# Optimization experiments

Measured on AMD Instinct MI355X. Metric: run time of the kernel, lower is better.

## Reference

```python
import jax, jax.numpy as jnp
import numpy as np

B = 32          # number of trees (batch)
N_LEAVES = 512  # complete binary tree -> 2*N_LEAVES-1 nodes per tree
IN_DIM = 1024
MEM = 1024


def setup_inputs() -> dict:
    key = jax.random.key(0)
    k1, k2, k3, k4 = jax.random.split(key, 4)
    s = 0.02
    inputs = jax.random.normal(k1, (B, N_LEAVES, IN_DIM), jnp.float32)
    w_fioux = jax.random.normal(k2, (4 * MEM, IN_DIM), jnp.float32) * s
    # rand_init: bias zero except first mem_dim entries set to 1 (forget-gate bias)
    b_fioux = jnp.zeros((4 * MEM,), jnp.float32).at[:MEM].set(1.0)
    w_iouh = jax.random.normal(k3, (3 * MEM, 2 * MEM), jnp.float32) * s
    w_fh = jax.random.normal(k4, (2 * MEM, 2 * MEM), jnp.float32) * s
    return {"inputs": inputs, "w_fioux": w_fioux, "b_fioux": b_fioux,
            "w_iouh": w_iouh, "w_fh": w_fh}


def _node_forward(x, child_c, child_h, w_fioux, b_fioux, w_iouh, w_fh):
    # x: [B, n, IN_DIM]; child_c/child_h: [B, n, 2*MEM] (left || right)
    fioux = x @ w_fioux.T + b_fioux                      # [B, n, 4M]
    fx, ix, ox, ux = jnp.split(fioux, 4, axis=-1)        # each [B, n, M]
    ih, oh, uh = jnp.split(child_h @ w_iouh.T, 3, axis=-1)
    i = jax.nn.sigmoid(ix + ih)
    o = jax.nn.sigmoid(ox + oh)
    u = jnp.tanh(ux + uh)
    # f gates: fx repeated for both children + fh(child_h)
    f = jax.nn.sigmoid(jnp.concatenate([fx, fx], axis=-1) + child_h @ w_fh.T)
    fc = f * child_c                                     # [B, n, 2M]
    c = i * u + fc[..., :MEM] + fc[..., MEM:]            # sum over the 2 children
    h = o * jnp.tanh(c)
    return c, h


def reference(inputs, w_fioux, b_fioux, w_iouh, w_fh):
    # Leaves: x = word input, child states are zeros
    z = jnp.zeros((B, N_LEAVES, 2 * MEM), inputs.dtype)
    c, h = _node_forward(inputs, z, z, w_fioux, b_fioux, w_iouh, w_fh)
    n = N_LEAVES
    # Internal nodes, level by level (log2(N_LEAVES) fixed iterations):
    # x = zeros (internal nodes have no token input), children are adjacent pairs.
    while n > 1:
        n //= 2
        child_c = c.reshape(B, n, 2 * MEM)   # [left_c || right_c]
        child_h = h.reshape(B, n, 2 * MEM)
        x = jnp.zeros((B, n, IN_DIM), inputs.dtype)
        c, h = _node_forward(x, child_c, child_h, w_fioux, b_fioux, w_iouh, w_fh)
    return h[:, 0, :]  # root hidden state, [B, MEM]
```

## Files before the change

kernel.cpp:

```cpp
#include <hip/hip_runtime.h>
#include <cstdint>
#include <cstddef>


typedef __attribute__((ext_vector_type(8))) short bf16x8;
typedef __attribute__((ext_vector_type(4))) float f32x4;

__device__ __forceinline__ float sig_(float x) { return 1.0f / (1.0f + __expf(-x)); }

__device__ __forceinline__ unsigned short f2bf_(float x) {
    union { float f; uint32_t u; } v; v.f = x;
    uint32_t r = v.u + 0x7fffu + ((v.u >> 16) & 1u);
    return (unsigned short)(r >> 16);
}
__device__ __forceinline__ float bf2f_(unsigned short u) {
    union { uint32_t u; float f; } v; v.u = ((uint32_t)u) << 16; return v.f;
}

#define GL16(g, l) __builtin_amdgcn_global_load_lds( \
    (const __attribute__((address_space(1))) void*)(g), \
    (__attribute__((address_space(3))) void*)(l), 16, 0, 0)

__global__ __launch_bounds__(512, 2)
void gemm256(const unsigned short* __restrict__ A,
             const unsigned short* __restrict__ W,
             unsigned short* __restrict__ C, int M, int N, int lda, int Klen)
{
    __shared__ unsigned short lA[4 * 8192];
    __shared__ unsigned short lB[4 * 8192];

    const int gx = gridDim.x, gy = gridDim.y;
    int id = blockIdx.x + gx * (blockIdx.y + gy * blockIdx.z);
    {
        const int nwg = gx * gy * gridDim.z;
        const int q = nwg >> 3, r = nwg & 7, x = id & 7, i = id >> 3;
        id = (x < r ? x * (q + 1) : r * (q + 1) + (x - r) * q) + i;
    }
    const int bz  = id / (gx * gy);
    const int rem = id - bz * gx * gy;
    const int by  = rem / gx;
    const int bx  = rem - by * gx;

    const int tid = threadIdx.x;
    const int ln  = tid & 63;
    const int wv  = tid >> 6;
    const int wrp = wv >> 2;
    const int wcp = wv & 3;
    const int row0 = by * 256;
    const int colb = bx * 256;
    const int kbase = bz * Klen;
    C += (size_t)bz * M * N;

    const int rowS = tid >> 2;
    const int gS   = (tid & 3) ^ ((tid >> 3) & 3);
    const unsigned short* a0 = A + (size_t)min(row0 + rowS,       M - 1) * lda + kbase + gS * 8;
    const unsigned short* a1 = A + (size_t)min(row0 + rowS + 128, M - 1) * lda + kbase + gS * 8;
    const unsigned short* b0 = W + (size_t)(colb + rowS)       * lda + kbase + gS * 8;
    const unsigned short* b1 = W + (size_t)(colb + rowS + 128) * lda + kbase + gS * 8;
    const int ld0 = tid * 8;
    const int ld1 = tid * 8 + 4096;

    int offA[8], offB[4];
    #pragma unroll
    for (int i = 0; i < 8; ++i) {
        const int r = wrp * 128 + i * 16 + (ln & 15);
        offA[i] = r * 32 + ((ln >> 4) ^ ((r >> 1) & 3)) * 8;
    }
    #pragma unroll
    for (int i = 0; i < 4; ++i) {
        const int r = wcp * 64 + i * 16 + (ln & 15);
        offB[i] = r * 32 + ((ln >> 4) ^ ((r >> 1) & 3)) * 8;
    }

    f32x4 acc[8][4] = {};
    const int NT = Klen >> 6;

#define ISSUE_KH(kh) do { \
    const int _sl = (kh) & 3; \
    const size_t _ko = (size_t)(kh) * 32; \
    GL16(a0 + _ko, lA + _sl * 8192 + ld0); \
    GL16(a1 + _ko, lA + _sl * 8192 + ld1); \
    GL16(b0 + _ko, lB + _sl * 8192 + ld0); \
    GL16(b1 + _ko, lB + _sl * 8192 + ld1); \
} while (0)

#define PHASE(SLOT, KH, DOISS, WAITN, DOBAR) do { \
    const unsigned short* _pa = lA + (SLOT) * 8192; \
    const unsigned short* _pb = lB + (SLOT) * 8192; \
    bf16x8 _af[8], _bf[4]; \
    _Pragma("unroll") for (int _i = 0; _i < 4; ++_i) _bf[_i] = *(const bf16x8*)(_pb + offB[_i]); \
    _Pragma("unroll") for (int _i = 0; _i < 4; ++_i) _af[_i] = *(const bf16x8*)(_pa + offA[_i]); \
    if (DOISS) ISSUE_KH(KH); \
    __builtin_amdgcn_s_setprio(1); \
    _Pragma("unroll") for (int _m = 0; _m < 4; ++_m) \
        _Pragma("unroll") for (int _n = 0; _n < 4; ++_n) \
            acc[_m][_n] = __builtin_amdgcn_mfma_f32_16x16x32_bf16(_af[_m], _bf[_n], acc[_m][_n], 0, 0, 0); \
    __builtin_amdgcn_s_setprio(0); \
    _Pragma("unroll") for (int _i = 4; _i < 8; ++_i) _af[_i] = *(const bf16x8*)(_pa + offA[_i]); \
    __builtin_amdgcn_s_setprio(1); \
    _Pragma("unroll") for (int _m = 4; _m < 8; ++_m) \
        _Pragma("unroll") for (int _n = 0; _n < 4; ++_n) \
            acc[_m][_n] = __builtin_amdgcn_mfma_f32_16x16x32_bf16(_af[_m], _bf[_n], acc[_m][_n], 0, 0, 0); \
    __builtin_amdgcn_s_setprio(0); \
    if ((WAITN) == 8)      asm volatile("s_waitcnt vmcnt(8)" ::: "memory"); \
    else if ((WAITN) == 4) asm volatile("s_waitcnt vmcnt(4)" ::: "memory"); \
    else if ((WAITN) == 0) asm volatile("s_waitcnt vmcnt(0)" ::: "memory"); \
    if (DOBAR) asm volatile("s_barrier" ::: "memory"); \
} while (0)

    ISSUE_KH(0); ISSUE_KH(1); ISSUE_KH(2);
    asm volatile("s_waitcnt vmcnt(8)" ::: "memory");
    asm volatile("s_barrier" ::: "memory");

    for (int t = 0; t <= NT - 3; ++t) {
        const int ph = 2 * t;
        PHASE((ph) & 3,     ph + 3, 1, 8, 1);
        PHASE((ph + 1) & 3, ph + 4, 1, 8, 1);
    }
    {
        const int ph = 2 * NT - 4;
        PHASE((ph) & 3,     ph + 3, 1,  8, 1);
        PHASE((ph + 1) & 3, 0,      0,  4, 1);
        PHASE((ph + 2) & 3, 0,      0,  0, 1);
        PHASE((ph + 3) & 3, 0,      0, -1, 0);
    }
#undef PHASE
#undef ISSUE_KH

    #pragma unroll
    for (int mi = 0; mi < 8; ++mi) {
        #pragma unroll
        for (int ni = 0; ni < 4; ++ni) {
            const int col = colb + wcp * 64 + ni * 16 + (ln & 15);
            #pragma unroll
            for (int rg = 0; rg < 4; ++rg) {
                const int r = row0 + wrp * 128 + mi * 16 + (ln >> 4) * 4 + rg;
                if (r < M) C[(size_t)r * N + col] = f2bf_(acc[mi][ni][rg]);
            }
        }
    }
}

__global__ void f2bf_vec(const float* __restrict__ src, unsigned short* __restrict__ dst, int n4)
{
    const int i = blockIdx.x * blockDim.x + threadIdx.x;
    if (i >= n4) return;
    const float4 v = ((const float4*)src)[i];
    ushort4 o;
    o.x = f2bf_(v.x); o.y = f2bf_(v.y); o.z = f2bf_(v.z); o.w = f2bf_(v.w);
    ((ushort4*)dst)[i] = o;
}

__global__ void leaf_gates(const unsigned short* __restrict__ g, const float* __restrict__ b,
                           unsigned short* __restrict__ c_out, unsigned short* __restrict__ h_out,
                           int rows)
{
    const int idx = blockIdx.x * blockDim.x + threadIdx.x;
    if (idx >= rows * 256) return;
    const int r = idx >> 8, q = (idx & 255) << 2;
    const unsigned short* gr = g + (size_t)r * 3072;
    const ushort4 ix = *(const ushort4*)(gr + q);
    const ushort4 ox = *(const ushort4*)(gr + 1024 + q);
    const ushort4 ux = *(const ushort4*)(gr + 2048 + q);
    const float* bi = b + 1024 + q;
    const float* bo = b + 2048 + q;
    const float* bu = b + 3072 + q;
    ushort4 co, ho;
    const float c0 = sig_(bf2f_(ix.x) + bi[0]) * tanhf(bf2f_(ux.x) + bu[0]);
    const float c1 = sig_(bf2f_(ix.y) + bi[1]) * tanhf(bf2f_(ux.y) + bu[1]);
    const float c2 = sig_(bf2f_(ix.z) + bi[2]) * tanhf(bf2f_(ux.z) + bu[2]);
    const float c3 = sig_(bf2f_(ix.w) + bi[3]) * tanhf(bf2f_(ux.w) + bu[3]);
    co.x = f2bf_(c0); co.y = f2bf_(c1); co.z = f2bf_(c2); co.w = f2bf_(c3);
    ho.x = f2bf_(sig_(bf2f_(ox.x) + bo[0]) * tanhf(c0));
    ho.y = f2bf_(sig_(bf2f_(ox.y) + bo[1]) * tanhf(c1));
    ho.z = f2bf_(sig_(bf2f_(ox.z) + bo[2]) * tanhf(c2));
    ho.w = f2bf_(sig_(bf2f_(ox.w) + bo[3]) * tanhf(c3));
    *(ushort4*)(c_out + (size_t)r * 1024 + q) = co;
    *(ushort4*)(h_out + (size_t)r * 1024 + q) = ho;
}

__device__ __forceinline__ void acc4_(float* v, ushort4 u) {
    v[0] += bf2f_(u.x); v[1] += bf2f_(u.y); v[2] += bf2f_(u.z); v[3] += bf2f_(u.w);
}

__global__ void node_gates(const unsigned short* __restrict__ g, int S, size_t sstride,
                           const float* __restrict__ b,
                           const unsigned short* __restrict__ c_prev,
                           unsigned short* __restrict__ c_out,
                           unsigned short* __restrict__ h_bf,
                           float* __restrict__ h_f32, int rows)
{
    const int idx = blockIdx.x * blockDim.x + threadIdx.x;
    if (idx >= rows * 256) return;
    const int r = idx >> 8, q = (idx & 255) << 2;
    float vi[4] = {}, vo[4] = {}, vu[4] = {}, vfl[4] = {}, vfr[4] = {};
    const unsigned short* gr = g + (size_t)r * 5120 + q;
    for (int s = 0; s < S; ++s, gr += sstride) {
        acc4_(vi,  *(const ushort4*)(gr));
        acc4_(vo,  *(const ushort4*)(gr + 1024));
        acc4_(vu,  *(const ushort4*)(gr + 2048));
        acc4_(vfl, *(const ushort4*)(gr + 3072));
        acc4_(vfr, *(const ushort4*)(gr + 4096));
    }
    const float* bi = b + 1024 + q;
    const float* bo = b + 2048 + q;
    const float* bu = b + 3072 + q;
    const float* bff = b + q;
    const ushort4 clu = *(const ushort4*)(c_prev + (size_t)r * 2048 + q);
    const ushort4 cru = *(const ushort4*)(c_prev + (size_t)r * 2048 + 1024 + q);
    const float cl[4] = { bf2f_(clu.x), bf2f_(clu.y), bf2f_(clu.z), bf2f_(clu.w) };
    const float cr[4] = { bf2f_(cru.x), bf2f_(cru.y), bf2f_(cru.z), bf2f_(cru.w) };

    ushort4 co, ho;
    float hv[4];
    float cv[4];
    #pragma unroll
    for (int e = 0; e < 4; ++e) {
        const float c = sig_(vi[e] + bi[e]) * tanhf(vu[e] + bu[e])
                      + sig_(vfl[e] + bff[e]) * cl[e]
                      + sig_(vfr[e] + bff[e]) * cr[e];
        cv[e] = c;
        hv[e] = sig_(vo[e] + bo[e]) * tanhf(c);
    }
    co.x = f2bf_(cv[0]); co.y = f2bf_(cv[1]); co.z = f2bf_(cv[2]); co.w = f2bf_(cv[3]);
    ho.x = f2bf_(hv[0]); ho.y = f2bf_(hv[1]); ho.z = f2bf_(hv[2]); ho.w = f2bf_(hv[3]);
    *(ushort4*)(c_out + (size_t)r * 1024 + q) = co;
    *(ushort4*)(h_bf + (size_t)r * 1024 + q) = ho;
    if (h_f32) {
        float4 hf; hf.x = hv[0]; hf.y = hv[1]; hf.z = hv[2]; hf.w = hv[3];
        *(float4*)(h_f32 + (size_t)r * 1024 + q) = hf;
    }
}

extern "C" void kernel_launch(void* const* d_in, const int* in_sizes, int n_in,
                              void* d_out, int out_size, void* d_ws, size_t ws_size,
                              hipStream_t stream)
{
    const float* inputs  = (const float*)d_in[0];
    const float* w_fioux = (const float*)d_in[1];
    const float* b_fioux = (const float*)d_in[2];
    const float* w_iouh  = (const float*)d_in[3];
    const float* w_fh    = (const float*)d_in[4];
    float* out = (float*)d_out;

    unsigned short* us   = (unsigned short*)d_ws;
    unsigned short* c_a  = us;
    unsigned short* c_b  = c_a + (size_t)16777216;
    unsigned short* h_a  = c_b + (size_t)8388608;
    unsigned short* h_b  = h_a + (size_t)16777216;
    unsigned short* wfx  = h_b + (size_t)8388608;
    unsigned short* wcat = wfx + (size_t)3145728;
    unsigned short* gbuf = wcat + (size_t)10485760;
    unsigned short* x_bf = c_a;

    f2bf_vec<<<16384, 256, 0, stream>>>(inputs, x_bf, 4194304);
    f2bf_vec<<<3072, 256, 0, stream>>>(w_fioux + (size_t)1024 * 1024, wfx, 786432);
    f2bf_vec<<<6144, 256, 0, stream>>>(w_iouh, wcat, 1572864);
    f2bf_vec<<<4096, 256, 0, stream>>>(w_fh, wcat + (size_t)3072 * 2048, 1048576);

    gemm256<<<dim3(12, 64, 1), 512, 0, stream>>>(x_bf, wfx, gbuf, 16384, 3072, 1024, 1024);
    leaf_gates<<<16384, 256, 0, stream>>>(gbuf, b_fioux, c_a, h_a, 16384);

    unsigned short *hp = h_a, *cp = c_a, *hn = h_b, *cn = c_b;
    for (int n = 256; n >= 1; n >>= 1) {
        const int m = 32 * n;
        int S;
        if (m >= 8192)      S = 1;
        else if (m >= 4096) S = 2;
        else if (m >= 2048) S = 1;
        else if (m >= 512)  S = 4;
        else                S = 8;
        const int Klen = 2048 / S;
        gemm256<<<dim3(20, (m + 255) / 256, S), 512, 0, stream>>>(
            hp, wcat, gbuf, m, 5120, 2048, Klen);
        node_gates<<<m, 256, 0, stream>>>(
            gbuf, S, (size_t)m * 5120, b_fioux, cp, cn, hn,
            (n == 1) ? out : nullptr, m);
        unsigned short* t;
        t = hp; hp = hn; hn = t;
        t = cp; cp = cn; cn = t;
    }
    (void)in_sizes; (void)n_in; (void)out_size; (void)ws_size;
}
```

Before: 784.0 us.

## Fuse gate epilogue into interleaved-weight GEMM for large tree levels

Adds a gemm320f kernel that uses 320-column tiles over a reordered weight matrix, so that each tile holds all five gate slices (i, o, u, f_left, f_right) for 64 hidden units. The LSTM cell update then runs directly in the GEMM epilogue for the large levels (n=256..64). This removes the bf16 gate buffer round trip and the separate node_gates launch for those levels. The remaining levels keep split-K gemm256 plus node_gates, with node_gates indexing the new interleaved layout. The gemm256 main loop is also restructured into a single per-32-K phase with explicit waits, barriers and sched_barriers, which shifts when the LDS waits happen relative to the MFMAs.

```diff
diff --git a/kernel.cpp b/kernel.cpp
--- a/kernel.cpp
+++ b/kernel.cpp
@@ -20,6 +20,15 @@
 #define GL16(g, l) __builtin_amdgcn_global_load_lds( \
     (const __attribute__((address_space(1))) void*)(g), \
     (__attribute__((address_space(3))) void*)(l), 16, 0, 0)
+
+#define PHASE_WAITS(p, P) do { \
+    if ((p) <= (P) - 4)      asm volatile("s_waitcnt vmcnt(8)" ::: "memory"); \
+    else if ((p) == (P) - 3) asm volatile("s_waitcnt vmcnt(4)" ::: "memory"); \
+    else if ((p) == (P) - 2) asm volatile("s_waitcnt vmcnt(0)" ::: "memory"); \
+    asm volatile("s_barrier" ::: "memory"); \
+    asm volatile("s_waitcnt lgkmcnt(0)" ::: "memory"); \
+    __builtin_amdgcn_sched_barrier(0); \
+} while (0)
 
 __global__ __launch_bounds__(512, 2)
 void gemm256(const unsigned short* __restrict__ A,
@@ -73,7 +82,7 @@
     }
 
     f32x4 acc[8][4] = {};
-    const int NT = Klen >> 6;
+    const int P = Klen >> 5;
 
 #define ISSUE_KH(kh) do { \
     const int _sl = (kh) & 3; \
@@ -84,47 +93,41 @@
     GL16(b1 + _ko, lB + _sl * 8192 + ld1); \
 } while (0)
 
-#define PHASE(SLOT, KH, DOISS, WAITN, DOBAR) do { \
-    const unsigned short* _pa = lA + (SLOT) * 8192; \
-    const unsigned short* _pb = lB + (SLOT) * 8192; \
-    bf16x8 _af[8], _bf[4]; \
-    _Pragma("unroll") for (int _i = 0; _i < 4; ++_i) _bf[_i] = *(const bf16x8*)(_pb + offB[_i]); \
-    _Pragma("unroll") for (int _i = 0; _i < 4; ++_i) _af[_i] = *(const bf16x8*)(_pa + offA[_i]); \
-    if (DOISS) ISSUE_KH(KH); \
-    __builtin_amdgcn_s_setprio(1); \
-    _Pragma("unroll") for (int _m = 0; _m < 4; ++_m) \
-        _Pragma("unroll") for (int _n = 0; _n < 4; ++_n) \
-            acc[_m][_n] = __builtin_amdgcn_mfma_f32_16x16x32_bf16(_af[_m], _bf[_n], acc[_m][_n], 0, 0, 0); \
-    __builtin_amdgcn_s_setprio(0); \
-    _Pragma("unroll") for (int _i = 4; _i < 8; ++_i) _af[_i] = *(const bf16x8*)(_pa + offA[_i]); \
-    __builtin_amdgcn_s_setprio(1); \
-    _Pragma("unroll") for (int _m = 4; _m < 8; ++_m) \
-        _Pragma("unroll") for (int _n = 0; _n < 4; ++_n) \
-            acc[_m][_n] = __builtin_amdgcn_mfma_f32_16x16x32_bf16(_af[_m], _bf[_n], acc[_m][_n], 0, 0, 0); \
-    __builtin_amdgcn_s_setprio(0); \
-    if ((WAITN) == 8)      asm volatile("s_waitcnt vmcnt(8)" ::: "memory"); \
-    else if ((WAITN) == 4) asm volatile("s_waitcnt vmcnt(4)" ::: "memory"); \
-    else if ((WAITN) == 0) asm volatile("s_waitcnt vmcnt(0)" ::: "memory"); \
-    if (DOBAR) asm volatile("s_barrier" ::: "memory"); \
-} while (0)
-
     ISSUE_KH(0); ISSUE_KH(1); ISSUE_KH(2);
     asm volatile("s_waitcnt vmcnt(8)" ::: "memory");
     asm volatile("s_barrier" ::: "memory");
 
-    for (int t = 0; t <= NT - 3; ++t) {
-        const int ph = 2 * t;
-        PHASE((ph) & 3,     ph + 3, 1, 8, 1);
-        PHASE((ph + 1) & 3, ph + 4, 1, 8, 1);
-    }
-    {
-        const int ph = 2 * NT - 4;
-        PHASE((ph) & 3,     ph + 3, 1,  8, 1);
-        PHASE((ph + 1) & 3, 0,      0,  4, 1);
-        PHASE((ph + 2) & 3, 0,      0,  0, 1);
-        PHASE((ph + 3) & 3, 0,      0, -1, 0);
-    }
-#undef PHASE
+    for (int p = 0; p < P; ++p) {
+        const unsigned short* pa = lA + (p & 3) * 8192;
+        const unsigned short* pb = lB + (p & 3) * 8192;
+        bf16x8 bf[4], af[4];
+        #pragma unroll
+        for (int i = 0; i < 4; ++i) bf[i] = *(const bf16x8*)(pb + offB[i]);
+        #pragma unroll
+        for (int i = 0; i < 4; ++i) af[i] = *(const bf16x8*)(pa + offA[i]);
+        if (p <= P - 4) ISSUE_KH(p + 3);
+        PHASE_WAITS(p, P);
+        __builtin_amdgcn_s_setprio(1);
+        #pragma unroll
+        for (int m = 0; m < 4; ++m)
+            #pragma unroll
+            for (int n = 0; n < 4; ++n)
+                acc[m][n] = __builtin_amdgcn_mfma_f32_16x16x32_bf16(af[m], bf[n], acc[m][n], 0, 0, 0);
+        __builtin_amdgcn_s_setprio(0);
+        bf16x8 ag[4];
+        #pragma unroll
+        for (int i = 0; i < 4; ++i) ag[i] = *(const bf16x8*)(pa + offA[4 + i]);
+        asm volatile("s_waitcnt lgkmcnt(0)" ::: "memory");
+        __builtin_amdgcn_sched_barrier(0);
+        __builtin_amdgcn_s_setprio(1);
+        #pragma unroll
+        for (int m = 0; m < 4; ++m)
+            #pragma unroll
+            for (int n = 0; n < 4; ++n)
+                acc[4 + m][n] = __builtin_amdgcn_mfma_f32_16x16x32_bf16(ag[m], bf[n], acc[4 + m][n], 0, 0, 0);
+        __builtin_amdgcn_s_setprio(0);
+        asm volatile("s_barrier" ::: "memory");
+    }
 #undef ISSUE_KH
 
     #pragma unroll
@@ -141,6 +144,137 @@
     }
 }
 
+__global__ __launch_bounds__(512, 2)
+void gemm320f(const unsigned short* __restrict__ A,
+              const unsigned short* __restrict__ Wp,
+              const float* __restrict__ b,
+              const unsigned short* __restrict__ c_prev,
+              unsigned short* __restrict__ c_out,
+              unsigned short* __restrict__ h_out,
+              int M)
+{
+    __shared__ unsigned short lA[4 * 8192];
+    __shared__ unsigned short lB[4 * 10240];
+    const int lda = 2048;
+
+    const int gx = gridDim.x, gy = gridDim.y;
+    int id = blockIdx.x + gx * blockIdx.y;
+    {
+        const int nwg = gx * gy;
+        const int q = nwg >> 3, r = nwg & 7, x = id & 7, i = id >> 3;
+        id = (x < r ? x * (q + 1) : r * (q + 1) + (x - r) * q) + i;
+    }
+    const int by = id / gx;
+    const int bx = id - by * gx;
+
+    const int tid = threadIdx.x;
+    const int ln  = tid & 63;
+    const int wv  = tid >> 6;
+    const int wrp = wv >> 2;
+    const int wcp = wv & 3;
+    const int row0 = by * 256;
+    const int colb = bx * 320;
+
+    const int rowS = tid >> 2;
+    const int gS   = (tid & 3) ^ ((tid >> 3) & 3);
+    const unsigned short* a0 = A + (size_t)min(row0 + rowS,       M - 1) * lda + gS * 8;
+    const unsigned short* a1 = A + (size_t)min(row0 + rowS + 128, M - 1) * lda + gS * 8;
+    const unsigned short* w0 = Wp + (size_t)(colb + rowS)       * lda + gS * 8;
+    const unsigned short* w1 = Wp + (size_t)(colb + rowS + 128) * lda + gS * 8;
+    const unsigned short* w2 = Wp + (size_t)(colb + 256 + ((tid & 255) >> 2)) * lda + gS * 8;
+    const int ld0 = tid * 8;
+    const int ld1 = tid * 8 + 4096;
+    const int ld2 = (tid & 255) * 8 + 8192;
+
+    int offA[8], offB[5];
+    #pragma unroll
+    for (int i = 0; i < 8; ++i) {
+        const int r = wrp * 128 + i * 16 + (ln & 15);
+        offA[i] = r * 32 + ((ln >> 4) ^ ((r >> 1) & 3)) * 8;
+    }
+    #pragma unroll
+    for (int g = 0; g < 5; ++g) {
+        const int r = g * 64 + wcp * 16 + (ln & 15);
+        offB[g] = r * 32 + ((ln >> 4) ^ ((r >> 1) & 3)) * 8;
+    }
+
+    f32x4 acc[8][5] = {};
+    const int P = 64;
+
+#define ISSUE_F(kh) do { \
+    const int _sl = (kh) & 3; \
+    const size_t _ko = (size_t)(kh) * 32; \
+    GL16(a0 + _ko, lA + _sl * 8192 + ld0); \
+    GL16(a1 + _ko, lA + _sl * 8192 + ld1); \
+    GL16(w0 + _ko, lB + _sl * 10240 + ld0); \
+    GL16(w1 + _ko, lB + _sl * 10240 + ld1); \
+    if (wv < 4) GL16(w2 + _ko, lB + _sl * 10240 + ld2); \
+} while (0)
+
+    ISSUE_F(0); ISSUE_F(1); ISSUE_F(2);
+    asm volatile("s_waitcnt vmcnt(8)" ::: "memory");
+    asm volatile("s_barrier" ::: "memory");
+
+    for (int p = 0; p < P; ++p) {
+        const unsigned short* pa = lA + (p & 3) * 8192;
+        const unsigned short* pb = lB + (p & 3) * 10240;
+        bf16x8 bf[5], af[4];
+        #pragma unroll
+        for (int g = 0; g < 5; ++g) bf[g] = *(const bf16x8*)(pb + offB[g]);
+        #pragma unroll
+        for (int i = 0; i < 4; ++i) af[i] = *(const bf16x8*)(pa + offA[i]);
+        if (p <= P - 4) ISSUE_F(p + 3);
+        PHASE_WAITS(p, P);
+        __builtin_amdgcn_s_setprio(1);
+        #pragma unroll
+        for (int m = 0; m < 4; ++m)
+            #pragma unroll
+            for (int g = 0; g < 5; ++g)
+                acc[m][g] = __builtin_amdgcn_mfma_f32_16x16x32_bf16(af[m], bf[g], acc[m][g], 0, 0, 0);
+        __builtin_amdgcn_s_setprio(0);
+        bf16x8 ag[4];
+        #pragma unroll
+        for (int i = 0; i < 4; ++i) ag[i] = *(const bf16x8*)(pa + offA[4 + i]);
+        asm volatile("s_waitcnt lgkmcnt(0)" ::: "memory");
+        __builtin_amdgcn_sched_barrier(0);
+        __builtin_amdgcn_s_setprio(1);
+        #pragma unroll
+        for (int m = 0; m < 4; ++m)
+            #pragma unroll
+            for (int g = 0; g < 5; ++g)
+                acc[4 + m][g] = __builtin_amdgcn_mfma_f32_16x16x32_bf16(ag[m], bf[g], acc[4 + m][g], 0, 0, 0);
+        __builtin_amdgcn_s_setprio(0);
+        asm volatile("s_barrier" ::: "memory");
+    }
+#undef ISSUE_F
+
+    const int jg = bx * 64 + wcp * 16 + (ln & 15);
+    const float bi = b[1024 + jg];
+    const float bo = b[2048 + jg];
+    const float bu = b[3072 + jg];
+    const float bff = b[jg];
+    #pragma unroll
+    for (int mi = 0; mi < 8; ++mi) {
+        #pragma unroll
+        for (int rg = 0; rg < 4; ++rg) {
+            const int r = row0 + wrp * 128 + mi * 16 + (ln >> 4) * 4 + rg;
+            if (r < M) {
+                const float cl = bf2f_(c_prev[(size_t)r * 2048 + jg]);
+                const float cr = bf2f_(c_prev[(size_t)r * 2048 + 1024 + jg]);
+                const float iv = sig_(acc[mi][0][rg] + bi);
+                const float ov = sig_(acc[mi][1][rg] + bo);
+                const float uv = tanhf(acc[mi][2][rg] + bu);
+                const float flv = sig_(acc[mi][3][rg] + bff);
+                const float frv = sig_(acc[mi][4][rg] + bff);
+                const float c = iv * uv + flv * cl + frv * cr;
+                const float h = ov * tanhf(c);
+                c_out[(size_t)r * 1024 + jg] = f2bf_(c);
+                h_out[(size_t)r * 1024 + jg] = f2bf_(h);
+            }
+        }
+    }
+}
+
 __global__ void f2bf_vec(const float* __restrict__ src, unsigned short* __restrict__ dst, int n4)
 {
     const int i = blockIdx.x * blockDim.x + threadIdx.x;
@@ -149,6 +283,26 @@
     ushort4 o;
     o.x = f2bf_(v.x); o.y = f2bf_(v.y); o.z = f2bf_(v.z); o.w = f2bf_(v.w);
     ((ushort4*)dst)[i] = o;
+}
+
+__global__ void build_wcatp(const float* __restrict__ w_iouh, const float* __restrict__ w_fh,
+                            unsigned short* __restrict__ dst, int total4)
+{
+    const int idx = blockIdx.x * blockDim.x + threadIdx.x;
+    if (idx >= total4) return;
+    const int rp = idx >> 9;
+    const int c4 = (idx & 511) << 2;
+    const int t  = rp / 320;
+    const int q  = rp - t * 320;
+    const int g  = q >> 6;
+    const int jj = q & 63;
+    const int srow = t * 64 + jj;
+    const float* src = (g < 3) ? (w_iouh + (size_t)(g * 1024 + srow) * 2048)
+                               : (w_fh   + (size_t)((g - 3) * 1024 + srow) * 2048);
+    const float4 v = *(const float4*)(src + c4);
+    ushort4 o;
+    o.x = f2bf_(v.x); o.y = f2bf_(v.y); o.z = f2bf_(v.z); o.w = f2bf_(v.w);
+    *(ushort4*)(dst + (size_t)rp * 2048 + c4) = o;
 }
 
 __global__ void leaf_gates(const unsigned short* __restrict__ g, const float* __restrict__ b,
@@ -193,14 +347,15 @@
     const int idx = blockIdx.x * blockDim.x + threadIdx.x;
     if (idx >= rows * 256) return;
     const int r = idx >> 8, q = (idx & 255) << 2;
+    const int t = q >> 6, jj = q & 63;
     float vi[4] = {}, vo[4] = {}, vu[4] = {}, vfl[4] = {}, vfr[4] = {};
-    const unsigned short* gr = g + (size_t)r * 5120 + q;
+    const unsigned short* gr = g + (size_t)r * 5120 + t * 320 + jj;
     for (int s = 0; s < S; ++s, gr += sstride) {
         acc4_(vi,  *(const ushort4*)(gr));
-        acc4_(vo,  *(const ushort4*)(gr + 1024));
-        acc4_(vu,  *(const ushort4*)(gr + 2048));
-        acc4_(vfl, *(const ushort4*)(gr + 3072));
-        acc4_(vfr, *(const ushort4*)(gr + 4096));
+        acc4_(vo,  *(const ushort4*)(gr + 64));
+        acc4_(vu,  *(const ushort4*)(gr + 128));
+        acc4_(vfl, *(const ushort4*)(gr + 192));
+        acc4_(vfr, *(const ushort4*)(gr + 256));
     }
     const float* bi = b + 1024 + q;
     const float* bo = b + 2048 + q;
@@ -212,8 +367,7 @@
     const float cr[4] = { bf2f_(cru.x), bf2f_(cru.y), bf2f_(cru.z), bf2f_(cru.w) };
 
     ushort4 co, ho;
-    float hv[4];
-    float cv[4];
+    float cv[4], hv[4];
     #pragma unroll
     for (int e = 0; e < 4; ++e) {
         const float c = sig_(vi[e] + bi[e]) * tanhf(vu[e] + bu[e])
@@ -243,36 +397,38 @@
     const float* w_fh    = (const float*)d_in[4];
     float* out = (float*)d_out;
 
-    unsigned short* us   = (unsigned short*)d_ws;
-    unsigned short* c_a  = us;
-    unsigned short* c_b  = c_a + (size_t)16777216;
-    unsigned short* h_a  = c_b + (size_t)8388608;
-    unsigned short* h_b  = h_a + (size_t)16777216;
-    unsigned short* wfx  = h_b + (size_t)8388608;
-    unsigned short* wcat = wfx + (size_t)3145728;
-    unsigned short* gbuf = wcat + (size_t)10485760;
-    unsigned short* x_bf = c_a;
+    unsigned short* us    = (unsigned short*)d_ws;
+    unsigned short* c_a   = us;
+    unsigned short* c_b   = c_a + (size_t)16777216;
+    unsigned short* h_a   = c_b + (size_t)8388608;
+    unsigned short* h_b   = h_a + (size_t)16777216;
+    unsigned short* wfx   = h_b + (size_t)8388608;
+    unsigned short* wcatP = wfx + (size_t)3145728;
+    unsigned short* gbuf  = wcatP + (size_t)10485760;
+    unsigned short* x_bf  = c_a;
 
     f2bf_vec<<<16384, 256, 0, stream>>>(inputs, x_bf, 4194304);
     f2bf_vec<<<3072, 256, 0, stream>>>(w_fioux + (size_t)1024 * 1024, wfx, 786432);
-    f2bf_vec<<<6144, 256, 0, stream>>>(w_iouh, wcat, 1572864);
-    f2bf_vec<<<4096, 256, 0, stream>>>(w_fh, wcat + (size_t)3072 * 2048, 1048576);
+    build_wcatp<<<10240, 256, 0, stream>>>(w_iouh, w_fh, wcatP, 5120 * 512);
 
     gemm256<<<dim3(12, 64, 1), 512, 0, stream>>>(x_bf, wfx, gbuf, 16384, 3072, 1024, 1024);
     leaf_gates<<<16384, 256, 0, stream>>>(gbuf, b_fioux, c_a, h_a, 16384);
 
     unsigned short *hp = h_a, *cp = c_a, *hn = h_b, *cn = c_b;
-    for (int n = 256; n >= 1; n >>= 1) {
+    for (int n = 256; n >= 64; n >>= 1) {
         const int m = 32 * n;
-        int S;
-        if (m >= 8192)      S = 1;
-        else if (m >= 4096) S = 2;
-        else if (m >= 2048) S = 1;
-        else if (m >= 512)  S = 4;
-        else                S = 8;
+        gemm320f<<<dim3(16, m / 256), 512, 0, stream>>>(hp, wcatP, b_fioux, cp, cn, hn, m);
+        unsigned short* t;
+        t = hp; hp = hn; hn = t;
+        t = cp; cp = cn; cn = t;
+    }
+
+    for (int n = 32; n >= 1; n >>= 1) {
+        const int m = 32 * n;
+        const int S = (m >= 512) ? 4 : 8;
         const int Klen = 2048 / S;
         gemm256<<<dim3(20, (m + 255) / 256, S), 512, 0, stream>>>(
-            hp, wcat, gbuf, m, 5120, 2048, Klen);
+            hp, wcatP, gbuf, m, 5120, 2048, Klen);
         node_gates<<<m, 256, 0, stream>>>(
             gbuf, S, (size_t)m * 5120, b_fioux, cp, cn, hn,
             (n == 1) ? out : nullptr, m);
```

Result: faster. 736.4 us (-6.1%).
